# Performance work log

Measured on AMD Instinct MI355X. Metric: run time of the kernel, lower is better.

Reference implementation:

```python
import jax, jax.numpy as jnp
import numpy as np

B, N, D = 8, 2048, 1024  # batch, seq_len, input_dim (= dim_k = dim_v)

def setup_inputs() -> dict:
    key = jax.random.key(0)
    k1, k2, k3, k4, k5 = jax.random.split(key, 5)
    s = 1.0 / np.sqrt(D)
    return {
        "img": jax.random.normal(k1, (B, N, D), dtype=jnp.float32),
        "text": jax.random.normal(k2, (B, N, D), dtype=jnp.float32),
        "Wq": jax.random.normal(k3, (D, D), dtype=jnp.float32) * s,
        "Wk": jax.random.normal(k4, (D, D), dtype=jnp.float32) * s,
        "Wv": jax.random.normal(k5, (D, D), dtype=jnp.float32) * s,
    }

def reference(img, text, Wq, Wk, Wv):
    # Linear layers (bias=False): y = x @ W^T (torch Linear convention)
    Q = jnp.einsum('bnd,kd->bnk', img, Wq)    # [B, N, dim_k]
    K = jnp.einsum('bmd,kd->bmk', text, Wk)   # [B, M, dim_k]
    V = jnp.einsum('bmd,vd->bmv', text, Wv)   # [B, M, dim_v]
    alpha_qk = jnp.einsum('bnk,bmk->bnm', Q, K)  # QK^T, no 1/sqrt(dk) scaling (as in source)
    alpha = jax.nn.softmax(alpha_qk, axis=1)     # softmax over QUERY axis (dim=1), as in source
    out = jnp.einsum('bnm,bmv->bnv', alpha, V)   # [B, N, dim_v]
    feature = out + text
    return (out, feature)
```

## Files before the change

### kernel.cpp

```cpp
#include <hip/hip_runtime.h>
#include <math.h>

#define B 8
#define N 2048
#define D 1024

#define BM 128
#define BN 128
#define BK 32

typedef __bf16 bf16;
typedef __bf16 bf16x8 __attribute__((ext_vector_type(8)));
typedef __bf16 bf16x4 __attribute__((ext_vector_type(4)));
typedef float f32x4 __attribute__((ext_vector_type(4)));

__device__ __forceinline__ void load_lds16(const void* g, void* l) {
    __builtin_amdgcn_global_load_lds((const __attribute__((address_space(1))) void*)g,
                                     (__attribute__((address_space(3))) void*)l, 16, 0, 0);
}

#define MFMA16(a, b, c) __builtin_amdgcn_mfma_f32_16x16x32_bf16(a, b, c, 0, 0, 0)
#define BARRIER() asm volatile("s_barrier" ::: "memory")
#define WAITV8() asm volatile("s_waitcnt vmcnt(8)" ::: "memory")
#define WAITV0() asm volatile("s_waitcnt vmcnt(0)" ::: "memory")

__global__ __launch_bounds__(256) void split_fp32(const float* __restrict__ x,
                                                  bf16* __restrict__ h,
                                                  bf16* __restrict__ l, long n)
{
    long i = ((long)blockIdx.x * 256 + threadIdx.x) * 4;
    if (i >= n) return;
    float4 v = *(const float4*)(x + i);
    float vs[4] = {v.x, v.y, v.z, v.w};
    bf16x4 hh, ll;
#pragma unroll
    for (int t = 0; t < 4; ++t) {
        bf16 hv = (bf16)vs[t];
        hh[t] = hv;
        ll[t] = (bf16)(vs[t] - (float)hv);
    }
    *(bf16x4*)(h + i) = hh;
    *(bf16x4*)(l + i) = ll;
}

__global__ __launch_bounds__(256) void tsplit_1024(const float* __restrict__ W,
                                                   bf16* __restrict__ WT_h,
                                                   bf16* __restrict__ WT_l)
{
    __shared__ float tile[64][65];
    const int d0 = blockIdx.x * 64, k0 = blockIdx.y * 64;
    const int tx = threadIdx.x & 63, ty = threadIdx.x >> 6;
#pragma unroll
    for (int r = 0; r < 16; ++r) {
        int kl = ty + r * 4;
        tile[kl][tx] = W[(size_t)(k0 + kl) * 1024 + d0 + tx];
    }
    __syncthreads();
#pragma unroll
    for (int r = 0; r < 16; ++r) {
        int dl = ty + r * 4;
        float v = tile[tx][dl];
        bf16 hv = (bf16)v;
        size_t idx = (size_t)(d0 + dl) * 1024 + k0 + tx;
        WT_h[idx] = hv;
        WT_l[idx] = (bf16)(v - (float)hv);
    }
}

template<int TERMS, int EPI>
__global__ __launch_bounds__(256) void gemm_nt_mfma(
    const bf16* __restrict__ Ah_g, const bf16* __restrict__ Al_g,
    const bf16* __restrict__ Bh_g, const bf16* __restrict__ Bl_g,
    bf16* __restrict__ Chi, bf16* __restrict__ Clo,
    float* __restrict__ Cf, const float* __restrict__ Text,
    float* __restrict__ Feat,
    int Mdim, int Ncdim, int Kdim, long sA, long sB, long sC)
{
    __shared__ bf16 Ah[BM][BK];
    __shared__ bf16 Bh[BN][BK];
    __shared__ bf16 Al[BM][BK];
    __shared__ bf16 Bl[BN][BK];

    const int tid = threadIdx.x;
    const int lane = tid & 63;
    const int wv = tid >> 6;
    const int wr = (wv >> 1) * 64;
    const int wc = (wv & 1) * 64;
    const int mfrag = lane & 15;
    const int quad = lane >> 4;

    const long z = blockIdx.z;
    const int row0 = blockIdx.y * BM;
    const int col0 = blockIdx.x * BN;

    const bf16* Abh = Ah_g + z * sA;
    const bf16* Abl = (TERMS == 3) ? (Al_g + z * sA) : nullptr;
    const bf16* Bbh = Bh_g + z * sB;
    const bf16* Bbl = (TERMS == 3) ? (Bl_g + z * sB) : nullptr;

    f32x4 acc[4][4] = {};

    for (int k0 = 0; k0 < Kdim; k0 += BK) {
#pragma unroll
        for (int q = 0; q < 2; ++q) {
            int c = q * 256 + tid;
            int row = c >> 2, kp = (c & 3) * 8;
            load_lds16(Abh + (long)(row0 + row) * Kdim + k0 + kp, &Ah[row][kp]);
            load_lds16(Bbh + (long)(col0 + row) * Kdim + k0 + kp, &Bh[row][kp]);
            if constexpr (TERMS == 3) {
                load_lds16(Abl + (long)(row0 + row) * Kdim + k0 + kp, &Al[row][kp]);
                load_lds16(Bbl + (long)(col0 + row) * Kdim + k0 + kp, &Bl[row][kp]);
            }
        }
        __syncthreads();

        bf16x8 a_h[4], b_h[4], a_l[4], b_l[4];
#pragma unroll
        for (int i = 0; i < 4; ++i) {
            a_h[i] = *(const bf16x8*)&Ah[wr + i * 16 + mfrag][quad * 8];
            b_h[i] = *(const bf16x8*)&Bh[wc + i * 16 + mfrag][quad * 8];
            if constexpr (TERMS == 3) {
                a_l[i] = *(const bf16x8*)&Al[wr + i * 16 + mfrag][quad * 8];
                b_l[i] = *(const bf16x8*)&Bl[wc + i * 16 + mfrag][quad * 8];
            }
        }
#pragma unroll
        for (int i = 0; i < 4; ++i)
#pragma unroll
            for (int j = 0; j < 4; ++j) {
                acc[i][j] = MFMA16(a_h[i], b_h[j], acc[i][j]);
                if constexpr (TERMS == 3) {
                    acc[i][j] = MFMA16(a_h[i], b_l[j], acc[i][j]);
                    acc[i][j] = MFMA16(a_l[i], b_h[j], acc[i][j]);
                }
            }
        __syncthreads();
    }

    const long cbase = z * sC;
    const bool wlo = (Clo != nullptr);
#pragma unroll
    for (int i = 0; i < 4; ++i) {
#pragma unroll
        for (int r = 0; r < 4; ++r) {
            int row = row0 + wr + i * 16 + quad * 4 + r;
#pragma unroll
            for (int j = 0; j < 4; ++j) {
                int col = col0 + wc + j * 16 + mfrag;
                long idx = cbase + (long)row * Ncdim + col;
                float v = acc[i][j][r];
                if constexpr (EPI == 0) {
                    bf16 h = (bf16)v;
                    Chi[idx] = h;
                    if (wlo) Clo[idx] = (bf16)(v - (float)h);
                } else if constexpr (EPI == 1) {
                    Cf[idx] = v;
                } else {
                    Cf[idx] = v;
                    Feat[idx] = v + Text[idx];
                }
            }
        }
    }
}


__device__ __forceinline__ void stage32(const bf16* __restrict__ g, int Kd, int k0,
                                        bf16* l, int tid)
{
#pragma unroll
    for (int c = 0; c < 2; ++c) {
        int idx = c * 512 + tid;
        int row = idx >> 2;
        int slot = idx & 3;
        int kk = ((slot ^ ((row >> 1) & 3)) << 3);
        load_lds16(g + (long)row * Kd + k0 + kk, l + (size_t)idx * 8);
    }
}

__device__ __forceinline__ void stage64(const bf16* __restrict__ g, int Kd, int k0,
                                        bf16* l, int tid)
{
#pragma unroll
    for (int c = 0; c < 4; ++c) {
        int idx = c * 512 + tid;
        int row = idx >> 3;
        int slot = idx & 7;
        int kk = ((slot ^ (row & 7)) << 3);
        load_lds16(g + (long)row * Kd + k0 + kk, l + (size_t)idx * 8);
    }
}

__device__ __forceinline__ bf16x8 rd32(const bf16* l, int row, int quad) {
    return *(const bf16x8*)(l + row * 32 + ((quad ^ ((row >> 1) & 3)) << 3));
}
__device__ __forceinline__ bf16x8 rd64(const bf16* l, int row, int ks, int quad) {
    return *(const bf16x8*)(l + row * 64 + (((ks * 4 + quad) ^ (row & 7)) << 3));
}

template<int EPI>
__global__ __launch_bounds__(512) void gemm256_3t(
    const bf16* __restrict__ Ah_g, const bf16* __restrict__ Al_g,
    const bf16* __restrict__ Bh_g, const bf16* __restrict__ Bl_g,
    bf16* __restrict__ Chi, bf16* __restrict__ Clo, float* __restrict__ Cf,
    int Ncdim, int Kdim, long sA, long sB, long sC)
{
    __shared__ __align__(16) bf16 lds[2][4][256 * 32];

    const int tid = threadIdx.x;
    const int lane = tid & 63;
    const int wv = tid >> 6;
    const int wrow = (wv >> 2) << 7;
    const int wcol = (wv & 3) << 6;
    const int mfrag = lane & 15;
    const int quad = lane >> 4;

    const long z = blockIdx.z;
    const int row0 = blockIdx.y * 256;
    const int col0 = blockIdx.x * 256;

    const bf16* Abh = Ah_g + z * sA + (long)row0 * Kdim;
    const bf16* Abl = Al_g + z * sA + (long)row0 * Kdim;
    const bf16* Bbh = Bh_g + z * sB + (long)col0 * Kdim;
    const bf16* Bbl = Bl_g + z * sB + (long)col0 * Kdim;

    f32x4 acc[8][4] = {};
    const int NT = Kdim >> 5;

    stage32(Abh, Kdim, 0, lds[0][0], tid);
    stage32(Abl, Kdim, 0, lds[0][1], tid);
    stage32(Bbh, Kdim, 0, lds[0][2], tid);
    stage32(Bbl, Kdim, 0, lds[0][3], tid);

    for (int t = 0; t < NT; ++t) {
        const int cur = t & 1;
        const bf16* LAh = lds[cur][0];
        const bf16* LAl = lds[cur][1];
        const bf16* LBh = lds[cur][2];
        const bf16* LBl = lds[cur][3];

        if (t + 1 < NT) {
            const int k0 = (t + 1) << 5;
            stage32(Abh, Kdim, k0, lds[cur ^ 1][0], tid);
            stage32(Abl, Kdim, k0, lds[cur ^ 1][1], tid);
            stage32(Bbh, Kdim, k0, lds[cur ^ 1][2], tid);
            stage32(Bbl, Kdim, k0, lds[cur ^ 1][3], tid);
            WAITV8();
        } else {
            WAITV0();
        }
        BARRIER();
        bf16x8 ah[8], bh[4];
#pragma unroll
        for (int i = 0; i < 8; ++i) ah[i] = rd32(LAh, wrow + i * 16 + mfrag, quad);
#pragma unroll
        for (int j = 0; j < 4; ++j) bh[j] = rd32(LBh, wcol + j * 16 + mfrag, quad);
        __builtin_amdgcn_s_setprio(1);
#pragma unroll
        for (int i = 0; i < 8; ++i)
#pragma unroll
            for (int j = 0; j < 4; ++j)
                acc[i][j] = MFMA16(ah[i], bh[j], acc[i][j]);
        __builtin_amdgcn_s_setprio(0);
        BARRIER();

        bf16x8 bl[4];
#pragma unroll
        for (int j = 0; j < 4; ++j) bl[j] = rd32(LBl, wcol + j * 16 + mfrag, quad);
        BARRIER();
        __builtin_amdgcn_s_setprio(1);
#pragma unroll
        for (int i = 0; i < 8; ++i)
#pragma unroll
            for (int j = 0; j < 4; ++j)
                acc[i][j] = MFMA16(ah[i], bl[j], acc[i][j]);
        __builtin_amdgcn_s_setprio(0);
        BARRIER();

        bf16x8 al[8];
#pragma unroll
        for (int i = 0; i < 8; ++i) al[i] = rd32(LAl, wrow + i * 16 + mfrag, quad);
        BARRIER();
        __builtin_amdgcn_s_setprio(1);
#pragma unroll
        for (int i = 0; i < 8; ++i)
#pragma unroll
            for (int j = 0; j < 4; ++j)
                acc[i][j] = MFMA16(al[i], bh[j], acc[i][j]);
        __builtin_amdgcn_s_setprio(0);
        BARRIER();
    }

    const long cbase = z * sC;
    const bool wlo = (Clo != nullptr);
#pragma unroll
    for (int i = 0; i < 8; ++i) {
#pragma unroll
        for (int r = 0; r < 4; ++r) {
            int row = row0 + wrow + i * 16 + quad * 4 + r;
            long rbase = cbase + (long)row * Ncdim;
#pragma unroll
            for (int j = 0; j < 4; ++j) {
                int col = col0 + wcol + j * 16 + mfrag;
                float v = acc[i][j][r];
                if constexpr (EPI == 0) {
                    bf16 h = (bf16)v;
                    Chi[rbase + col] = h;
                    if (wlo) Clo[rbase + col] = (bf16)(v - (float)h);
                } else {
                    Cf[rbase + col] = v;
                }
            }
        }
    }
}

template<int EPI>
__global__ __launch_bounds__(512) void gemm256_1t(
    const bf16* __restrict__ A_g, const bf16* __restrict__ B_g,
    bf16* __restrict__ Chi, float* __restrict__ Cf,
    const float* __restrict__ Text, float* __restrict__ Feat,
    int Ncdim, int Kdim, long sA, long sB, long sC)
{
    __shared__ __align__(16) bf16 lds[2][2][256 * 64];

    const int tid = threadIdx.x;
    const int lane = tid & 63;
    const int wv = tid >> 6;
    const int wrow = (wv >> 2) << 7;
    const int wcol = (wv & 3) << 6;
    const int mfrag = lane & 15;
    const int quad = lane >> 4;

    const long z = blockIdx.z;
    const int row0 = blockIdx.y * 256;
    const int col0 = blockIdx.x * 256;

    const bf16* Ab = A_g + z * sA + (long)row0 * Kdim;
    const bf16* Bb = B_g + z * sB + (long)col0 * Kdim;

    f32x4 acc[8][4] = {};
    const int NT = Kdim >> 6;

    stage64(Ab, Kdim, 0, lds[0][0], tid);
    stage64(Bb, Kdim, 0, lds[0][1], tid);

    for (int t = 0; t < NT; ++t) {
        const int cur = t & 1;
        const bf16* LA = lds[cur][0];
        const bf16* LB = lds[cur][1];

        if (t + 1 < NT) {
            const int k0 = (t + 1) << 6;
            stage64(Ab, Kdim, k0, lds[cur ^ 1][0], tid);
            stage64(Bb, Kdim, k0, lds[cur ^ 1][1], tid);
            WAITV8();
        } else {
            WAITV0();
        }
        BARRIER();
        bf16x8 a[4][2], b0[2][2], b1[2][2];
#pragma unroll
        for (int i = 0; i < 4; ++i)
#pragma unroll
            for (int ks = 0; ks < 2; ++ks)
                a[i][ks] = rd64(LA, wrow + i * 16 + mfrag, ks, quad);
#pragma unroll
        for (int j = 0; j < 2; ++j)
#pragma unroll
            for (int ks = 0; ks < 2; ++ks)
                b0[j][ks] = rd64(LB, wcol + j * 16 + mfrag, ks, quad);
        __builtin_amdgcn_s_setprio(1);
#pragma unroll
        for (int i = 0; i < 4; ++i)
#pragma unroll
            for (int j = 0; j < 2; ++j)
#pragma unroll
                for (int ks = 0; ks < 2; ++ks)
                    acc[i][j] = MFMA16(a[i][ks], b0[j][ks], acc[i][j]);
        __builtin_amdgcn_s_setprio(0);
        BARRIER();

#pragma unroll
        for (int j = 0; j < 2; ++j)
#pragma unroll
            for (int ks = 0; ks < 2; ++ks)
                b1[j][ks] = rd64(LB, wcol + (2 + j) * 16 + mfrag, ks, quad);
        BARRIER();
        __builtin_amdgcn_s_setprio(1);
#pragma unroll
        for (int i = 0; i < 4; ++i)
#pragma unroll
            for (int j = 0; j < 2; ++j)
#pragma unroll
                for (int ks = 0; ks < 2; ++ks)
                    acc[i][2 + j] = MFMA16(a[i][ks], b1[j][ks], acc[i][2 + j]);
        __builtin_amdgcn_s_setprio(0);
        BARRIER();

#pragma unroll
        for (int i = 0; i < 4; ++i)
#pragma unroll
            for (int ks = 0; ks < 2; ++ks)
                a[i][ks] = rd64(LA, wrow + (4 + i) * 16 + mfrag, ks, quad);
        BARRIER();
        __builtin_amdgcn_s_setprio(1);
#pragma unroll
        for (int i = 0; i < 4; ++i)
#pragma unroll
            for (int j = 0; j < 2; ++j)
#pragma unroll
                for (int ks = 0; ks < 2; ++ks)
                    acc[4 + i][2 + j] = MFMA16(a[i][ks], b1[j][ks], acc[4 + i][2 + j]);
        __builtin_amdgcn_s_setprio(0);
        BARRIER();

#pragma unroll
        for (int j = 0; j < 2; ++j)
#pragma unroll
            for (int ks = 0; ks < 2; ++ks)
                b0[j][ks] = rd64(LB, wcol + j * 16 + mfrag, ks, quad);
        BARRIER();
        __builtin_amdgcn_s_setprio(1);
#pragma unroll
        for (int i = 0; i < 4; ++i)
#pragma unroll
            for (int j = 0; j < 2; ++j)
#pragma unroll
                for (int ks = 0; ks < 2; ++ks)
                    acc[4 + i][j] = MFMA16(a[i][ks], b0[j][ks], acc[4 + i][j]);
        __builtin_amdgcn_s_setprio(0);
        BARRIER();
    }

    const long cbase = z * sC;
#pragma unroll
    for (int i = 0; i < 8; ++i) {
#pragma unroll
        for (int r = 0; r < 4; ++r) {
            int row = row0 + wrow + i * 16 + quad * 4 + r;
            long rbase = cbase + (long)row * Ncdim;
#pragma unroll
            for (int j = 0; j < 4; ++j) {
                int col = col0 + wcol + j * 16 + mfrag;
                float v = acc[i][j][r];
                if constexpr (EPI == 0) {
                    Chi[rbase + col] = (bf16)v;
                } else {
                    Cf[rbase + col] = v;
                    Feat[rbase + col] = v + Text[rbase + col];
                }
            }
        }
    }
}

__global__ __launch_bounds__(1024) void col_softmax_bf16(const float* __restrict__ S,
                                                         bf16* __restrict__ Aout)
{
    const int b = blockIdx.x / (N / 64);
    const int mbase = (blockIdx.x % (N / 64)) * 64;
    const int t = threadIdx.x;
    const int mloc = t & 63;
    const int slice = t >> 6;
    const int m = mbase + mloc;
    const float* Sb = S + (size_t)b * N * N;
    bf16* Ab = Aout + (size_t)b * N * N;
    const int n_lo = slice * (N / 16), n_hi = n_lo + (N / 16);

    __shared__ float red_m[16][64];
    __shared__ float red_s[16][64];

    float mx = -INFINITY, s = 0.0f;
    for (int n = n_lo; n < n_hi; n += 8) {
        float x[8];
#pragma unroll
        for (int u = 0; u < 8; ++u) x[u] = Sb[(size_t)(n + u) * N + m];
        float bm = x[0];
#pragma unroll
        for (int u = 1; u < 8; ++u) bm = fmaxf(bm, x[u]);
        float nm = fmaxf(mx, bm);
        float a = 0.0f;
#pragma unroll
        for (int u = 0; u < 8; ++u) a += __expf(x[u] - nm);
        s = s * __expf(mx - nm) + a;
        mx = nm;
    }
    red_m[slice][mloc] = mx;
    red_s[slice][mloc] = s;
    __syncthreads();

    float gm = -INFINITY;
#pragma unroll
    for (int i = 0; i < 16; ++i) gm = fmaxf(gm, red_m[i][mloc]);
    float den = 0.0f;
#pragma unroll
    for (int i = 0; i < 16; ++i) den += red_s[i][mloc] * __expf(red_m[i][mloc] - gm);
    float inv = 1.0f / den;

    for (int n = n_lo; n < n_hi; n += 8) {
        float x[8];
#pragma unroll
        for (int u = 0; u < 8; ++u) x[u] = Sb[(size_t)(n + u) * N + m];
#pragma unroll
        for (int u = 0; u < 8; ++u)
            Ab[(size_t)(n + u) * N + m] = (bf16)(__expf(x[u] - gm) * inv);
    }
}

extern "C" void kernel_launch(void* const* d_in, const int* in_sizes, int n_in,
                              void* d_out, int out_size, void* d_ws, size_t ws_size,
                              hipStream_t stream)
{
    const float* img  = (const float*)d_in[0];
    const float* text = (const float*)d_in[1];
    const float* Wq   = (const float*)d_in[2];
    const float* Wk   = (const float*)d_in[3];
    const float* Wv   = (const float*)d_in[4];

    const long E  = (long)B * N * D;
    const long W2 = (long)D * D;
    const long EN = (long)B * N * N;

    char* ws = (char*)d_ws;
    float* S     = (float*)ws;
    bf16* img_h  = (bf16*)ws;
    bf16* img_l  = img_h + E;
    bf16* WqT_h  = (bf16*)(ws + (size_t)4 * E);
    bf16* WqT_l  = WqT_h + W2;
    bf16* WkT_h  = WqT_l + W2;
    bf16* WkT_l  = WkT_h + W2;
    bf16* Wqk_h  = WkT_l + W2;
    bf16* Wqk_l  = Wqk_h + W2;
    bf16* Wv_l_s = Wqk_l + W2;
    float* out_pv = (float*)ws;

    bf16* text_h = (bf16*)(ws + (size_t)EN * 4);
    bf16* text_l = text_h + E;
    bf16* VT_h   = text_l;

    bf16* T_h  = (bf16*)d_out;
    bf16* T_l  = T_h + E;
    bf16* Wv_h = T_l + E;
    bf16* alpha = (bf16*)d_out;
    float* out  = (float*)d_out;
    float* feat = out + E;

    dim3 blk(256);
    dim3 blk5(512);

    split_fp32<<<E / 1024, blk, 0, stream>>>(img,  img_h,  img_l,  E);
    split_fp32<<<E / 1024, blk, 0, stream>>>(text, text_h, text_l, E);
    split_fp32<<<W2 / 1024, blk, 0, stream>>>(Wv, Wv_h, Wv_l_s, W2);
    tsplit_1024<<<dim3(16, 16), blk, 0, stream>>>(Wq, WqT_h, WqT_l);
    tsplit_1024<<<dim3(16, 16), blk, 0, stream>>>(Wk, WkT_h, WkT_l);

    gemm_nt_mfma<3, 0><<<dim3(8, 8, 1), blk, 0, stream>>>(
        WkT_h, WkT_l, WqT_h, WqT_l, Wqk_h, Wqk_l, nullptr, nullptr, nullptr,
        D, D, D, 0, 0, 0);

    gemm256_3t<0><<<dim3(D / 256, (B * N) / 256, 1), blk5, 0, stream>>>(
        img_h, img_l, Wqk_h, Wqk_l, T_h, T_l, nullptr,
        D, D, 0, 0, 0);

    gemm256_3t<1><<<dim3(N / 256, N / 256, B), blk5, 0, stream>>>(
        T_h, T_l, text_h, text_l, nullptr, nullptr, S,
        N, D, (long)N * D, (long)N * D, (long)N * N);

    gemm256_1t<0><<<dim3(N / 256, D / 256, B), blk5, 0, stream>>>(
        Wv_h, text_h, VT_h, nullptr, nullptr, nullptr,
        N, D, 0, (long)N * D, (long)D * N);

    col_softmax_bf16<<<dim3(B * N / 64), dim3(1024), 0, stream>>>(S, alpha);

    gemm256_1t<2><<<dim3(D / 256, N / 256, B), blk5, 0, stream>>>(
        alpha, VT_h, nullptr, out_pv, text, feat,
        N * 0 + D, N, (long)N * N, (long)D * N, (long)N * D);

    hipMemcpyAsync(out, out_pv, (size_t)E * 4, hipMemcpyDeviceToDevice, stream);
}
```

Before: 771.3 us.

## Interleave next-tile prefetch with MFMA phases, drop barriers, add XCD block swizzle

Both GEMM kernels now issue the global-to-LDS prefetch of the next K tile in pieces between MFMA groups instead of all at the start of an iteration. They also drop the per-phase barriers, keeping one wait and barrier at the top of each iteration. The register fragments are restructured so each phase reads only the LDS slices it needs. Block indices are remapped so consecutive tiles land on the same XCD, which should improve L2 reuse. The aim is to cut barrier stalls and hide load latency, at the cost of a full vmcnt(0) wait each iteration and some extra register pressure.

```diff
diff --git a/kernel.cpp b/kernel.cpp
--- a/kernel.cpp
+++ b/kernel.cpp
@@ -21,7 +21,6 @@
 
 #define MFMA16(a, b, c) __builtin_amdgcn_mfma_f32_16x16x32_bf16(a, b, c, 0, 0, 0)
 #define BARRIER() asm volatile("s_barrier" ::: "memory")
-#define WAITV8() asm volatile("s_waitcnt vmcnt(8)" ::: "memory")
 #define WAITV0() asm volatile("s_waitcnt vmcnt(0)" ::: "memory")
 
 __global__ __launch_bounds__(256) void split_fp32(const float* __restrict__ x,
@@ -165,6 +164,14 @@
 }
 
 
+__device__ __forceinline__ void xcd_swz(int& bx, int& by, int gx, int gy) {
+    int nwg = gx * gy;
+    int flat = by * gx + bx;
+    flat = (flat & 7) * (nwg >> 3) + (flat >> 3);
+    bx = flat % gx;
+    by = flat / gx;
+}
+
 __device__ __forceinline__ void stage32(const bf16* __restrict__ g, int Kd, int k0,
                                         bf16* l, int tid)
 {
@@ -216,8 +223,10 @@
     const int quad = lane >> 4;
 
     const long z = blockIdx.z;
-    const int row0 = blockIdx.y * 256;
-    const int col0 = blockIdx.x * 256;
+    int bx = blockIdx.x, by = blockIdx.y;
+    xcd_swz(bx, by, gridDim.x, gridDim.y);
+    const int row0 = by * 256;
+    const int col0 = bx * 256;
 
     const bf16* Abh = Ah_g + z * sA + (long)row0 * Kdim;
     const bf16* Abl = Al_g + z * sA + (long)row0 * Kdim;
@@ -228,8 +237,8 @@
     const int NT = Kdim >> 5;
 
     stage32(Abh, Kdim, 0, lds[0][0], tid);
+    stage32(Bbh, Kdim, 0, lds[0][2], tid);
     stage32(Abl, Kdim, 0, lds[0][1], tid);
-    stage32(Bbh, Kdim, 0, lds[0][2], tid);
     stage32(Bbl, Kdim, 0, lds[0][3], tid);
 
     for (int t = 0; t < NT; ++t) {
@@ -238,57 +247,70 @@
         const bf16* LAl = lds[cur][1];
         const bf16* LBh = lds[cur][2];
         const bf16* LBl = lds[cur][3];
-
-        if (t + 1 < NT) {
-            const int k0 = (t + 1) << 5;
-            stage32(Abh, Kdim, k0, lds[cur ^ 1][0], tid);
-            stage32(Abl, Kdim, k0, lds[cur ^ 1][1], tid);
-            stage32(Bbh, Kdim, k0, lds[cur ^ 1][2], tid);
-            stage32(Bbl, Kdim, k0, lds[cur ^ 1][3], tid);
-            WAITV8();
-        } else {
-            WAITV0();
-        }
+        const bool pf = (t + 1 < NT);
+        const int kn = (t + 1) << 5;
+
+        WAITV0();
         BARRIER();
-        bf16x8 ah[8], bh[4];
+
+        bf16x8 ah[8], bh[4], bl[4], al[8];
 #pragma unroll
         for (int i = 0; i < 8; ++i) ah[i] = rd32(LAh, wrow + i * 16 + mfrag, quad);
 #pragma unroll
         for (int j = 0; j < 4; ++j) bh[j] = rd32(LBh, wcol + j * 16 + mfrag, quad);
-        __builtin_amdgcn_s_setprio(1);
-#pragma unroll
-        for (int i = 0; i < 8; ++i)
+
+        __builtin_amdgcn_s_setprio(1);
+#pragma unroll
+        for (int i = 0; i < 4; ++i)
 #pragma unroll
             for (int j = 0; j < 4; ++j)
                 acc[i][j] = MFMA16(ah[i], bh[j], acc[i][j]);
         __builtin_amdgcn_s_setprio(0);
-        BARRIER();
-
-        bf16x8 bl[4];
+
+        if (pf) { stage32(Abh, Kdim, kn, lds[cur ^ 1][0], tid);
+                  stage32(Bbh, Kdim, kn, lds[cur ^ 1][2], tid); }
+
 #pragma unroll
         for (int j = 0; j < 4; ++j) bl[j] = rd32(LBl, wcol + j * 16 + mfrag, quad);
-        BARRIER();
-        __builtin_amdgcn_s_setprio(1);
-#pragma unroll
-        for (int i = 0; i < 8; ++i)
+
+        __builtin_amdgcn_s_setprio(1);
+#pragma unroll
+        for (int i = 4; i < 8; ++i)
+#pragma unroll
+            for (int j = 0; j < 4; ++j)
+                acc[i][j] = MFMA16(ah[i], bh[j], acc[i][j]);
+        __builtin_amdgcn_s_setprio(0);
+
+#pragma unroll
+        for (int i = 0; i < 4; ++i) al[i] = rd32(LAl, wrow + i * 16 + mfrag, quad);
+
+        __builtin_amdgcn_s_setprio(1);
+#pragma unroll
+        for (int i = 0; i < 4; ++i)
 #pragma unroll
             for (int j = 0; j < 4; ++j)
                 acc[i][j] = MFMA16(ah[i], bl[j], acc[i][j]);
         __builtin_amdgcn_s_setprio(0);
-        BARRIER();
-
-        bf16x8 al[8];
-#pragma unroll
-        for (int i = 0; i < 8; ++i) al[i] = rd32(LAl, wrow + i * 16 + mfrag, quad);
-        BARRIER();
-        __builtin_amdgcn_s_setprio(1);
+
+        if (pf) { stage32(Abl, Kdim, kn, lds[cur ^ 1][1], tid);
+                  stage32(Bbl, Kdim, kn, lds[cur ^ 1][3], tid); }
+
+#pragma unroll
+        for (int i = 4; i < 8; ++i) al[i] = rd32(LAl, wrow + i * 16 + mfrag, quad);
+
+        __builtin_amdgcn_s_setprio(1);
+#pragma unroll
+        for (int i = 4; i < 8; ++i)
+#pragma unroll
+            for (int j = 0; j < 4; ++j)
+                acc[i][j] = MFMA16(ah[i], bl[j], acc[i][j]);
+
 #pragma unroll
         for (int i = 0; i < 8; ++i)
 #pragma unroll
             for (int j = 0; j < 4; ++j)
                 acc[i][j] = MFMA16(al[i], bh[j], acc[i][j]);
         __builtin_amdgcn_s_setprio(0);
-        BARRIER();
     }
 
     const long cbase = z * sC;
@@ -333,8 +355,10 @@
     const int quad = lane >> 4;
 
     const long z = blockIdx.z;
-    const int row0 = blockIdx.y * 256;
-    const int col0 = blockIdx.x * 256;
+    int bx = blockIdx.x, by = blockIdx.y;
+    xcd_swz(bx, by, gridDim.x, gridDim.y);
+    const int row0 = by * 256;
+    const int col0 = bx * 256;
 
     const bf16* Ab = A_g + z * sA + (long)row0 * Kdim;
     const bf16* Bb = B_g + z * sB + (long)col0 * Kdim;
@@ -349,17 +373,13 @@
         const int cur = t & 1;
         const bf16* LA = lds[cur][0];
         const bf16* LB = lds[cur][1];
-
-        if (t + 1 < NT) {
-            const int k0 = (t + 1) << 6;
-            stage64(Ab, Kdim, k0, lds[cur ^ 1][0], tid);
-            stage64(Bb, Kdim, k0, lds[cur ^ 1][1], tid);
-            WAITV8();
-        } else {
-            WAITV0();
-        }
+        const bool pf = (t + 1 < NT);
+        const int kn = (t + 1) << 6;
+
+        WAITV0();
         BARRIER();
-        bf16x8 a[4][2], b0[2][2], b1[2][2];
+
+        bf16x8 a[8][2], b[4][2];
 #pragma unroll
         for (int i = 0; i < 4; ++i)
 #pragma unroll
@@ -369,7 +389,8 @@
         for (int j = 0; j < 2; ++j)
 #pragma unroll
             for (int ks = 0; ks < 2; ++ks)
-                b0[j][ks] = rd64(LB, wcol + j * 16 + mfrag, ks, quad);
+                b[j][ks] = rd64(LB, wcol + j * 16 + mfrag, ks, quad);
+
         __builtin_amdgcn_s_setprio(1);
 #pragma unroll
         for (int i = 0; i < 4; ++i)
@@ -377,60 +398,54 @@
             for (int j = 0; j < 2; ++j)
 #pragma unroll
                 for (int ks = 0; ks < 2; ++ks)
-                    acc[i][j] = MFMA16(a[i][ks], b0[j][ks], acc[i][j]);
-        __builtin_amdgcn_s_setprio(0);
-        BARRIER();
-
-#pragma unroll
-        for (int j = 0; j < 2; ++j)
+                    acc[i][j] = MFMA16(a[i][ks], b[j][ks], acc[i][j]);
+        __builtin_amdgcn_s_setprio(0);
+
+        if (pf) stage64(Ab, Kdim, kn, lds[cur ^ 1][0], tid);
+
+#pragma unroll
+        for (int j = 2; j < 4; ++j)
 #pragma unroll
             for (int ks = 0; ks < 2; ++ks)
-                b1[j][ks] = rd64(LB, wcol + (2 + j) * 16 + mfrag, ks, quad);
-        BARRIER();
+                b[j][ks] = rd64(LB, wcol + j * 16 + mfrag, ks, quad);
+
         __builtin_amdgcn_s_setprio(1);
 #pragma unroll
         for (int i = 0; i < 4; ++i)
 #pragma unroll
+            for (int j = 2; j < 4; ++j)
+#pragma unroll
+                for (int ks = 0; ks < 2; ++ks)
+                    acc[i][j] = MFMA16(a[i][ks], b[j][ks], acc[i][j]);
+        __builtin_amdgcn_s_setprio(0);
+
+#pragma unroll
+        for (int i = 4; i < 8; ++i)
+#pragma unroll
+            for (int ks = 0; ks < 2; ++ks)
+                a[i][ks] = rd64(LA, wrow + i * 16 + mfrag, ks, quad);
+
+        __builtin_amdgcn_s_setprio(1);
+#pragma unroll
+        for (int i = 4; i < 8; ++i)
+#pragma unroll
+            for (int j = 2; j < 4; ++j)
+#pragma unroll
+                for (int ks = 0; ks < 2; ++ks)
+                    acc[i][j] = MFMA16(a[i][ks], b[j][ks], acc[i][j]);
+        __builtin_amdgcn_s_setprio(0);
+
+        if (pf) stage64(Bb, Kdim, kn, lds[cur ^ 1][1], tid);
+
+        __builtin_amdgcn_s_setprio(1);
+#pragma unroll
+        for (int i = 4; i < 8; ++i)
+#pragma unroll
             for (int j = 0; j < 2; ++j)
 #pragma unroll
                 for (int ks = 0; ks < 2; ++ks)
-                    acc[i][2 + j] = MFMA16(a[i][ks], b1[j][ks], acc[i][2 + j]);
-        __builtin_amdgcn_s_setprio(0);
-        BARRIER();
-
-#pragma unroll
-        for (int i = 0; i < 4; ++i)
-#pragma unroll
-            for (int ks = 0; ks < 2; ++ks)
-                a[i][ks] = rd64(LA, wrow + (4 + i) * 16 + mfrag, ks, quad);
-        BARRIER();
-        __builtin_amdgcn_s_setprio(1);
-#pragma unroll
-        for (int i = 0; i < 4; ++i)
-#pragma unroll
-            for (int j = 0; j < 2; ++j)
-#pragma unroll
-                for (int ks = 0; ks < 2; ++ks)
-                    acc[4 + i][2 + j] = MFMA16(a[i][ks], b1[j][ks], acc[4 + i][2 + j]);
-        __builtin_amdgcn_s_setprio(0);
-        BARRIER();
-
-#pragma unroll
-        for (int j = 0; j < 2; ++j)
-#pragma unroll
-            for (int ks = 0; ks < 2; ++ks)
-                b0[j][ks] = rd64(LB, wcol + j * 16 + mfrag, ks, quad);
-        BARRIER();
-        __builtin_amdgcn_s_setprio(1);
-#pragma unroll
-        for (int i = 0; i < 4; ++i)
-#pragma unroll
-            for (int j = 0; j < 2; ++j)
-#pragma unroll
-                for (int ks = 0; ks < 2; ++ks)
-                    acc[4 + i][j] = MFMA16(a[i][ks], b0[j][ks], acc[4 + i][j]);
-        __builtin_amdgcn_s_setprio(0);
-        BARRIER();
+                    acc[i][j] = MFMA16(a[i][ks], b[j][ks], acc[i][j]);
+        __builtin_amdgcn_s_setprio(0);
     }
 
     const long cbase = z * sC;
@@ -575,7 +590,7 @@
 
     gemm256_1t<2><<<dim3(D / 256, N / 256, B), blk5, 0, stream>>>(
         alpha, VT_h, nullptr, out_pv, text, feat,
-        N * 0 + D, N, (long)N * N, (long)D * N, (long)N * D);
+        D, N, (long)N * N, (long)D * N, (long)N * D);
 
     hipMemcpyAsync(out, out_pv, (size_t)E * 4, hipMemcpyDeviceToDevice, stream);
 }
```

New measurement: 738.0 us. 4.3% less time.
